# Kernel optimization log

Measured on AMD Instinct MI355X. Metric: run time of the kernel, lower is better.

Reference implementation:

```python
import jax, jax.numpy as jnp
import numpy as np

B, K, D_MODEL = 4, 8400, 512
H, Q, V = 8, 64, 64
WIN, PAD = 168, 42
STEP = WIN - 2 * PAD  # 84


def setup_inputs() -> dict:
    key = jax.random.key(0)
    ks = jax.random.split(key, 11)
    s = 0.02
    return {
        "query": jax.random.normal(ks[0], (B, K, D_MODEL), jnp.float32),
        "key":   jax.random.normal(ks[1], (B, K, D_MODEL), jnp.float32),
        "value": jax.random.normal(ks[2], (B, K, D_MODEL), jnp.float32),
        "W_q": jax.random.normal(ks[3], (D_MODEL, Q * H), jnp.float32) * s,
        "b_q": jax.random.normal(ks[4], (Q * H,), jnp.float32) * s,
        "W_k": jax.random.normal(ks[5], (D_MODEL, Q * H), jnp.float32) * s,
        "b_k": jax.random.normal(ks[6], (Q * H,), jnp.float32) * s,
        "W_v": jax.random.normal(ks[7], (D_MODEL, V * H), jnp.float32) * s,
        "b_v": jax.random.normal(ks[8], (V * H,), jnp.float32) * s,
        "W_o": jax.random.normal(ks[9], (H * V, D_MODEL), jnp.float32) * s,
        "b_o": jax.random.normal(ks[10], (D_MODEL,), jnp.float32) * s,
    }


def _heads(x, d):
    # torch.cat(x.chunk(h, -1), dim=0): (B, Kp, h*d) -> (h*B, Kp, d), head-major
    b, kp, _ = x.shape
    return jnp.transpose(x.reshape(b, kp, H, d), (2, 0, 1, 3)).reshape(H * b, kp, d)


def reference(query, key, value, W_q, b_q, W_k, b_k, W_v, b_v, W_o, b_o):
    b = query.shape[0]
    # replicate padding along time axis
    pad = lambda x: jnp.pad(x, ((0, 0), (PAD, PAD), (0, 0)), mode="edge")
    qp, kp_, vp = pad(query), pad(key), pad(value)

    Qh = _heads(qp @ W_q + b_q, Q)   # (hB, Kp, Q)
    Kh = _heads(kp_ @ W_k + b_k, Q)
    Vh = _heads(vp @ W_v + b_v, V)

    n_win = K // STEP  # 100
    widx = jnp.arange(n_win)[:, None] * STEP + jnp.arange(WIN)[None, :]
    Qw = Qh[:, widx, :]
    Kw = Kh[:, widx, :]
    Vw = Vh[:, widx, :]

    scores = jnp.einsum("bnwq,bnxq->bnwx", Qw, Kw) / np.sqrt(WIN).astype(np.float32)
    tri = jnp.triu(jnp.ones((WIN, WIN), bool), 1)  # subsequent mask
    scores = jnp.where(tri, -jnp.inf, scores)
    attn_w = jax.nn.softmax(scores, axis=-1)
    attn = jnp.einsum("bnwx,bnxv->bnwv", attn_w, Vw)

    attn = attn[:, :, PAD:WIN - PAD, :]                      # crop padding
    attn = attn.reshape(H, b, n_win * STEP, V)               # (h, B, K, V)
    heads = jnp.transpose(attn, (1, 2, 0, 3)).reshape(b, K, H * V)
    return heads @ W_o + b_o
```

## Files before the change

kernel.cpp:

```cpp
#include <hip/hip_runtime.h>
#include <hip/hip_bf16.h>
#include <stdint.h>

#define BATCH 4
#define SEQ   8400
#define DM    512
#define KP    8484
#define NWIN  100
#define STEP_ 84
#define PAD_  42
#define NKEY  126
#define MROWS 33600

typedef __attribute__((ext_vector_type(8))) short short8;
typedef __attribute__((ext_vector_type(4))) float float4v;
typedef __attribute__((ext_vector_type(4))) unsigned short ushort4v;

#define MFMA16 __builtin_amdgcn_mfma_f32_16x16x32_bf16

__device__ __forceinline__ unsigned short f2bf(float f) {
    union { float f; unsigned u; } v; v.f = f;
    return (unsigned short)((v.u + 0x7FFFu + ((v.u >> 16) & 1u)) >> 16);
}
__device__ __forceinline__ unsigned short bfc(float f) {
    __hip_bfloat16 h = __float2bfloat16(f);
    union { __hip_bfloat16 h; unsigned short u; } v; v.h = h;
    return v.u;
}

typedef __attribute__((address_space(1))) const unsigned int as1_cu32;
typedef __attribute__((address_space(3))) unsigned int as3_u32;
__device__ __forceinline__ void gload16(const void* g, void* l) {
    __builtin_amdgcn_global_load_lds((as1_cu32*)g, (as3_u32*)l, 16, 0, 0);
}

__global__ __launch_bounds__(256) void kprep(const float* __restrict__ Wq,
                                             const float* __restrict__ Wk,
                                             const float* __restrict__ Wv,
                                             const float* __restrict__ Wo,
                                             unsigned short* __restrict__ Wt) {
    const float* src = blockIdx.z == 0 ? Wq : blockIdx.z == 1 ? Wk
                     : blockIdx.z == 2 ? Wv : Wo;
    unsigned short* dst = Wt + (size_t)blockIdx.z * DM * DM;
    __shared__ float t[64][65];
    int c = threadIdx.x & 63, r4 = threadIdx.x >> 6;
    int kb = blockIdx.x * 64, nb = blockIdx.y * 64;
    for (int i = 0; i < 16; i++) {
        int r = r4 * 16 + i;
        t[r][c] = src[(size_t)(kb + r) * DM + nb + c];
    }
    __syncthreads();
    for (int i = 0; i < 16; i++) {
        int r = r4 * 16 + i;
        dst[(size_t)(nb + r) * DM + kb + c] = f2bf(t[c][r]);
    }
}

__global__ __launch_bounds__(256, 2) void kproj(const float* __restrict__ q,
                                                const float* __restrict__ k,
                                                const float* __restrict__ v,
                                                const unsigned short* __restrict__ Wt,
                                                const float* __restrict__ bq,
                                                const float* __restrict__ bk,
                                                const float* __restrict__ bv,
                                                unsigned short* __restrict__ Qb,
                                                unsigned short* __restrict__ Kb,
                                                unsigned short* __restrict__ VT) {
    int mt = blockIdx.x, z = blockIdx.y;
    int ten = z >> 2, b = z & 3;
    const float* A = (ten == 0 ? q : ten == 1 ? k : v) + (size_t)b * SEQ * DM;
    const unsigned short* W = Wt + (size_t)ten * DM * DM;
    const float* bias = ten == 0 ? bq : ten == 1 ? bk : bv;
    float scale = ten == 0 ? 0.07715167498104595f : 1.f;
    int m0 = mt * 64;

    __shared__ __align__(16) char lds[81920];

    int tid = threadIdx.x, lane = tid & 63, wc = tid >> 6;
    int l15 = lane & 15, g = lane >> 4;

    float4v acc[4][8];
#pragma unroll
    for (int i = 0; i < 4; i++)
#pragma unroll
        for (int j = 0; j < 8; j++) { float4v zz = {0.f,0.f,0.f,0.f}; acc[i][j] = zz; }

    for (int kt = 0; kt < 8; kt++) {
#pragma unroll
        for (int it = 0; it < 4; it++) {
            int c = it * 256 + tid;
            int r = c >> 4;
            int c4 = (c & 15) ^ (r & 15);
            int p = m0 + r; if (p > KP - 1) p = KP - 1;
            int row = p - PAD_; row = row < 0 ? 0 : (row > SEQ - 1 ? SEQ - 1 : row);
            gload16(A + (size_t)row * DM + kt * 64 + c4 * 4,
                    lds + it * 4096 + wc * 1024);
        }
#pragma unroll
        for (int it = 0; it < 16; it++) {
            int c = it * 256 + tid;
            int r = c >> 3;
            int kg = (c & 7) ^ (r & 7);
            gload16(W + (size_t)r * DM + kt * 64 + kg * 8,
                    lds + 16384 + it * 4096 + wc * 1024);
        }
        __syncthreads();
#pragma unroll
        for (int ks = 0; ks < 2; ks++) {
            short8 af[4];
#pragma unroll
            for (int i = 0; i < 4; i++) {
                int r = i * 16 + l15;
                int c4a = (ks * 4 + g) * 2;
                float4v f0 = *(const float4v*)(lds + r * 256 + ((c4a ^ l15) << 4));
                float4v f1 = *(const float4v*)(lds + r * 256 + (((c4a + 1) ^ l15) << 4));
                short8 hv;
                hv[0] = (short)bfc(f0.x); hv[1] = (short)bfc(f0.y);
                hv[2] = (short)bfc(f0.z); hv[3] = (short)bfc(f0.w);
                hv[4] = (short)bfc(f1.x); hv[5] = (short)bfc(f1.y);
                hv[6] = (short)bfc(f1.z); hv[7] = (short)bfc(f1.w);
                af[i] = hv;
            }
            short8 bfr[8];
#pragma unroll
            for (int j = 0; j < 8; j++) {
                int r = wc * 128 + j * 16 + l15;
                int kg = ks * 4 + g;
                bfr[j] = *(const short8*)(lds + 16384 + r * 128 + ((kg ^ (r & 7)) << 4));
            }
#pragma unroll
            for (int i = 0; i < 4; i++)
#pragma unroll
                for (int j = 0; j < 8; j++)
                    acc[i][j] = MFMA16(af[i], bfr[j], acc[i][j], 0, 0, 0);
        }
        __syncthreads();
    }

    if (ten <= 1) {
        unsigned short* Ol = (unsigned short*)lds;
#pragma unroll
        for (int j = 0; j < 8; j++) {
            int n = wc * 128 + j * 16 + l15;
            float bval = bias[n];
#pragma unroll
            for (int i = 0; i < 4; i++) {
                float4v vv = acc[i][j];
#pragma unroll
                for (int r = 0; r < 4; r++)
                    Ol[(i * 16 + g * 4 + r) * 520 + n] = f2bf((vv[r] + bval) * scale);
            }
        }
        __syncthreads();
        unsigned short* O = ten == 0 ? Qb : Kb;
        for (int c = tid; c < 4096; c += 256) {
            int row = c >> 6, n8 = c & 63;
            int p = m0 + row;
            if (p < KP) {
                int h = n8 >> 3, ch = n8 & 7;
                *(short8*)(O + ((size_t)(h * BATCH + b) * KP + p) * 64 + ch * 8) =
                    *(const short8*)(Ol + row * 520 + n8 * 8);
            }
        }
    } else {
#pragma unroll
        for (int j = 0; j < 8; j++) {
            int n = wc * 128 + j * 16 + l15;
            float bval = bias[n];
            int h = n >> 6, d = n & 63;
            unsigned short* base = VT + ((size_t)(h * BATCH + b) * 64 + d) * KP;
#pragma unroll
            for (int i = 0; i < 4; i++) {
                int p = m0 + i * 16 + g * 4;
                if (p <= KP - 4) {
                    float4v vv = acc[i][j];
                    ushort4v wv;
                    wv[0] = f2bf(vv.x + bval); wv[1] = f2bf(vv.y + bval);
                    wv[2] = f2bf(vv.z + bval); wv[3] = f2bf(vv.w + bval);
                    *(ushort4v*)(base + p) = wv;
                }
            }
        }
    }
}

__global__ __launch_bounds__(384) void kattn(const unsigned short* __restrict__ Qb,
                                             const unsigned short* __restrict__ Kb,
                                             const unsigned short* __restrict__ VT,
                                             unsigned short* __restrict__ attn) {
    int win = blockIdx.x, hb = blockIdx.y;
    int h = hb >> 2, b = hb & 3;
    const unsigned short* Qg = Qb + (size_t)hb * KP * 64;
    const unsigned short* Kg = Kb + (size_t)hb * KP * 64;
    const unsigned short* Vt = VT + (size_t)hb * 64 * KP;
    int p0 = win * STEP_;

    __shared__ __align__(16) char lds[69632];

    int tid = threadIdx.x, lane = tid & 63, f = tid >> 6;
    int l15 = lane & 15, g = lane >> 4;

#pragma unroll
    for (int it = 0; it < 5; it++) {
        int base = it * 384 + f * 64;
        if (base < 768) {
            int c = base + lane;
            int qi = c >> 3, kg = (c & 7) ^ (qi & 7);
            gload16(Qg + (size_t)(p0 + PAD_ + qi) * 64 + kg * 8, lds + base * 16);
        } else if (base < 1792) {
            int c = base + lane - 768;
            int x = c >> 3, kg = (c & 7) ^ (x & 7);
            gload16(Kg + (size_t)(p0 + x) * 64 + kg * 8, lds + base * 16);
        }
    }
    for (int c = tid; c < 2048; c += 384) {
        int d = c >> 5, c2 = c & 31;
        ushort4v wv = *(const ushort4v*)(Vt + (size_t)d * KP + p0 + c2 * 4);
        int cx = c2 >> 1;
        *(ushort4v*)(lds + 28672 + d * 256 + (((cx ^ (d & 7)) << 4) | ((c2 & 1) * 8))) = wv;
    }
    __syncthreads();

    short8 bq2[2];
    {
        int r = f * 16 + l15;
#pragma unroll
        for (int ks = 0; ks < 2; ks++) {
            int kg = ks * 4 + g;
            bq2[ks] = *(const short8*)(lds + r * 128 + ((kg ^ (r & 7)) << 4));
        }
    }
    float4v st[8];
#pragma unroll
    for (int xf = 0; xf < 8; xf++) {
        float4v zz = {0.f,0.f,0.f,0.f}; st[xf] = zz;
#pragma unroll
        for (int ks = 0; ks < 2; ks++) {
            int r = xf * 16 + l15;
            int kg = ks * 4 + g;
            short8 a = *(const short8*)(lds + 12288 + r * 128 + ((kg ^ (r & 7)) << 4));
            st[xf] = MFMA16(a, bq2[ks], st[xf], 0, 0, 0);
        }
    }

    int w_abs = PAD_ + f * 16 + l15;
    int w_eff = w_abs > 125 ? 125 : w_abs;
    float mx = -1e30f;
#pragma unroll
    for (int xf = 0; xf < 8; xf++)
#pragma unroll
        for (int r = 0; r < 4; r++) {
            int x = xf * 16 + g * 4 + r;
            float vv = st[xf][r];
            if (x > w_eff) vv = -1e30f;
            st[xf][r] = vv;
            mx = fmaxf(mx, vv);
        }
    mx = fmaxf(mx, __shfl_xor(mx, 16));
    mx = fmaxf(mx, __shfl_xor(mx, 32));
    float s = 0.f;
#pragma unroll
    for (int xf = 0; xf < 8; xf++)
#pragma unroll
        for (int r = 0; r < 4; r++) {
            float e = __expf(st[xf][r] - mx);
            st[xf][r] = e;
            s += e;
        }
    s += __shfl_xor(s, 16);
    s += __shfl_xor(s, 32);
    float inv = 1.f / s;

    {
        int qi = f * 16 + l15;
#pragma unroll
        for (int xf = 0; xf < 8; xf++) {
            ushort4v pw;
#pragma unroll
            for (int r = 0; r < 4; r++) pw[r] = f2bf(st[xf][r] * inv);
            int xc = 2 * xf + (g >> 1);
            *(ushort4v*)(lds + 45056 + qi * 256 + ((xc ^ (qi & 7)) << 4) + (g & 1) * 8) = pw;
        }
    }
    __syncthreads();

    float4v pv[4];
#pragma unroll
    for (int j = 0; j < 4; j++) { float4v zz = {0.f,0.f,0.f,0.f}; pv[j] = zz; }
    int qi = f * 16 + l15;
#pragma unroll
    for (int g2 = 0; g2 < 4; g2++) {
        int xc = g2 * 4 + g;
        short8 a = *(const short8*)(lds + 45056 + qi * 256 + ((xc ^ (qi & 7)) << 4));
#pragma unroll
        for (int j = 0; j < 4; j++) {
            int d = j * 16 + l15;
            short8 bvv = *(const short8*)(lds + 28672 + d * 256 + ((xc ^ (d & 7)) << 4));
            pv[j] = MFMA16(a, bvv, pv[j], 0, 0, 0);
        }
    }

    unsigned short* Ol = (unsigned short*)lds;
#pragma unroll
    for (int j = 0; j < 4; j++) {
        int d = j * 16 + l15;
#pragma unroll
        for (int r = 0; r < 4; r++) {
            int qq = f * 16 + g * 4 + r;
            int byte = qq * 128 + ((((d >> 3) ^ (qq & 7))) << 4) + (d & 7) * 2;
            *(unsigned short*)((char*)Ol + byte) = f2bf(pv[j][r]);
        }
    }
    __syncthreads();
    for (int c = tid; c < 672; c += 384) {
        int qq = c >> 3, ch = c & 7;
        short8 hv = *(const short8*)((char*)Ol + qq * 128 + ((ch ^ (qq & 7)) << 4));
        size_t off = ((size_t)(b * SEQ + win * STEP_ + qq) * DM) + h * 64 + ch * 8;
        *(short8*)(attn + off) = hv;
    }
}

__global__ __launch_bounds__(256, 2) void kout(const unsigned short* __restrict__ Ab,
                                               const unsigned short* __restrict__ W,
                                               const float* __restrict__ bias,
                                               float* __restrict__ Out) {
    int m0 = blockIdx.x * 64;
    __shared__ __align__(16) char lds[73728];
    int tid = threadIdx.x, lane = tid & 63, wc = tid >> 6;
    int l15 = lane & 15, g = lane >> 4;

    float4v acc[4][8];
#pragma unroll
    for (int i = 0; i < 4; i++)
#pragma unroll
        for (int j = 0; j < 8; j++) { float4v zz = {0.f,0.f,0.f,0.f}; acc[i][j] = zz; }

    for (int kt = 0; kt < 8; kt++) {
#pragma unroll
        for (int it = 0; it < 2; it++) {
            int c = it * 256 + tid;
            int r = c >> 3;
            int kg = (c & 7) ^ (r & 7);
            gload16(Ab + (size_t)(m0 + r) * DM + kt * 64 + kg * 8,
                    lds + it * 4096 + wc * 1024);
        }
#pragma unroll
        for (int it = 0; it < 16; it++) {
            int c = it * 256 + tid;
            int r = c >> 3;
            int kg = (c & 7) ^ (r & 7);
            gload16(W + (size_t)r * DM + kt * 64 + kg * 8,
                    lds + 8192 + it * 4096 + wc * 1024);
        }
        __syncthreads();
#pragma unroll
        for (int ks = 0; ks < 2; ks++) {
            short8 af[4];
#pragma unroll
            for (int i = 0; i < 4; i++) {
                int r = i * 16 + l15;
                int kg = ks * 4 + g;
                af[i] = *(const short8*)(lds + r * 128 + ((kg ^ (r & 7)) << 4));
            }
            short8 bfr[8];
#pragma unroll
            for (int j = 0; j < 8; j++) {
                int r = wc * 128 + j * 16 + l15;
                int kg = ks * 4 + g;
                bfr[j] = *(const short8*)(lds + 8192 + r * 128 + ((kg ^ (r & 7)) << 4));
            }
#pragma unroll
            for (int i = 0; i < 4; i++)
#pragma unroll
                for (int j = 0; j < 8; j++)
                    acc[i][j] = MFMA16(af[i], bfr[j], acc[i][j], 0, 0, 0);
        }
        __syncthreads();
    }
#pragma unroll
    for (int j = 0; j < 8; j++) {
        int n = wc * 128 + j * 16 + l15;
        float bv = bias[n];
#pragma unroll
        for (int i = 0; i < 4; i++) {
            float4v vv = acc[i][j];
#pragma unroll
            for (int r = 0; r < 4; r++) {
                int m = m0 + i * 16 + g * 4 + r;
                Out[(size_t)m * DM + n] = vv[r] + bv;
            }
        }
    }
}

extern "C" void kernel_launch(void* const* d_in, const int* in_sizes, int n_in,
                              void* d_out, int out_size, void* d_ws, size_t ws_size,
                              hipStream_t stream) {
    const float* q  = (const float*)d_in[0];
    const float* k  = (const float*)d_in[1];
    const float* v  = (const float*)d_in[2];
    const float* Wq = (const float*)d_in[3];
    const float* bq = (const float*)d_in[4];
    const float* Wk = (const float*)d_in[5];
    const float* bk = (const float*)d_in[6];
    const float* Wv = (const float*)d_in[7];
    const float* bv = (const float*)d_in[8];
    const float* Wo = (const float*)d_in[9];
    const float* bo = (const float*)d_in[10];

    const size_t WT_ELEMS  = (size_t)4 * DM * DM;
    const size_t QKV_ELEMS = (size_t)32 * KP * 64;
    const size_t ATT_ELEMS = (size_t)MROWS * DM;
    size_t need = (WT_ELEMS + 3 * QKV_ELEMS + ATT_ELEMS) * 2;
    if (ws_size < need) return;

    unsigned short* Wt = (unsigned short*)d_ws;
    unsigned short* Qb = Wt + WT_ELEMS;
    unsigned short* Kb = Qb + QKV_ELEMS;
    unsigned short* VT = Kb + QKV_ELEMS;
    unsigned short* Ab = VT + QKV_ELEMS;

    kprep<<<dim3(8, 8, 4), dim3(256), 0, stream>>>(Wq, Wk, Wv, Wo, Wt);
    kproj<<<dim3(133, 12), dim3(256), 0, stream>>>(q, k, v, Wt, bq, bk, bv,
                                                   Qb, Kb, VT);
    kattn<<<dim3(NWIN, 32), dim3(384), 0, stream>>>(Qb, Kb, VT, Ab);
    kout<<<dim3(525), dim3(256), 0, stream>>>(Ab, Wt + 3 * DM * DM, bo,
                                              (float*)d_out);
}
```

Baseline: 229.5 us.

## Double-buffer LDS staging in projection GEMMs with async prefetch of next K-tile

Both the QKV projection kernel and the output projection kernel change from a single-buffered K loop (64-wide tiles, load then sync then compute) to a double-buffered pipeline with 32-wide K tiles. The next tile's global-to-LDS loads are issued before computing the current one, and partial vmcnt waits plus raw s_barrier replace full __syncthreads. The aim is to hide global load latency behind MFMA work. In exchange, K-steps double to 16, the LDS swizzle layout changes, and row clamping plus an output guard are added in kout.

```diff
diff --git a/kernel.cpp b/kernel.cpp
--- a/kernel.cpp
+++ b/kernel.cpp
@@ -85,56 +85,65 @@
 #pragma unroll
         for (int j = 0; j < 8; j++) { float4v zz = {0.f,0.f,0.f,0.f}; acc[i][j] = zz; }
 
-    for (int kt = 0; kt < 8; kt++) {
-#pragma unroll
-        for (int it = 0; it < 4; it++) {
+    auto stageA = [&](int kt, int buf) {
+#pragma unroll
+        for (int it = 0; it < 2; it++) {
             int c = it * 256 + tid;
-            int r = c >> 4;
-            int c4 = (c & 15) ^ (r & 15);
+            int r = c >> 3;
+            int pos = (c & 7) ^ (r & 7);
             int p = m0 + r; if (p > KP - 1) p = KP - 1;
             int row = p - PAD_; row = row < 0 ? 0 : (row > SEQ - 1 ? SEQ - 1 : row);
-            gload16(A + (size_t)row * DM + kt * 64 + c4 * 4,
-                    lds + it * 4096 + wc * 1024);
-        }
-#pragma unroll
-        for (int it = 0; it < 16; it++) {
+            gload16(A + (size_t)row * DM + kt * 32 + pos * 4,
+                    lds + buf * 8192 + (it * 256 + wc * 64) * 16);
+        }
+    };
+    auto stageB = [&](int kt, int buf) {
+#pragma unroll
+        for (int it = 0; it < 8; it++) {
             int c = it * 256 + tid;
-            int r = c >> 3;
-            int kg = (c & 7) ^ (r & 7);
-            gload16(W + (size_t)r * DM + kt * 64 + kg * 8,
-                    lds + 16384 + it * 4096 + wc * 1024);
-        }
-        __syncthreads();
-#pragma unroll
-        for (int ks = 0; ks < 2; ks++) {
-            short8 af[4];
-#pragma unroll
-            for (int i = 0; i < 4; i++) {
-                int r = i * 16 + l15;
-                int c4a = (ks * 4 + g) * 2;
-                float4v f0 = *(const float4v*)(lds + r * 256 + ((c4a ^ l15) << 4));
-                float4v f1 = *(const float4v*)(lds + r * 256 + (((c4a + 1) ^ l15) << 4));
-                short8 hv;
-                hv[0] = (short)bfc(f0.x); hv[1] = (short)bfc(f0.y);
-                hv[2] = (short)bfc(f0.z); hv[3] = (short)bfc(f0.w);
-                hv[4] = (short)bfc(f1.x); hv[5] = (short)bfc(f1.y);
-                hv[6] = (short)bfc(f1.z); hv[7] = (short)bfc(f1.w);
-                af[i] = hv;
-            }
-            short8 bfr[8];
-#pragma unroll
-            for (int j = 0; j < 8; j++) {
-                int r = wc * 128 + j * 16 + l15;
-                int kg = ks * 4 + g;
-                bfr[j] = *(const short8*)(lds + 16384 + r * 128 + ((kg ^ (r & 7)) << 4));
-            }
-#pragma unroll
-            for (int i = 0; i < 4; i++)
-#pragma unroll
-                for (int j = 0; j < 8; j++)
-                    acc[i][j] = MFMA16(af[i], bfr[j], acc[i][j], 0, 0, 0);
-        }
-        __syncthreads();
+            int r = c >> 2;
+            int pos = (c & 3) ^ ((r >> 1) & 3);
+            gload16(W + (size_t)r * DM + kt * 32 + pos * 8,
+                    lds + 16384 + buf * 32768 + (it * 256 + wc * 64) * 16);
+        }
+    };
+
+    stageA(0, 0); stageB(0, 0);
+#pragma unroll
+    for (int t = 0; t < 16; ++t) {
+        int cur = t & 1;
+        if (t < 15) { stageA(t + 1, cur ^ 1); stageB(t + 1, cur ^ 1); }
+        if (t < 15) asm volatile("s_waitcnt vmcnt(10)" ::: "memory");
+        else        asm volatile("s_waitcnt vmcnt(0)" ::: "memory");
+        __builtin_amdgcn_s_barrier();
+        __builtin_amdgcn_sched_barrier(0);
+        const char* Ab_ = lds + cur * 8192;
+        const char* Bb_ = lds + 16384 + cur * 32768;
+        short8 af[4];
+#pragma unroll
+        for (int i = 0; i < 4; i++) {
+            int ra = i * 16 + l15;
+            float4v f0 = *(const float4v*)(Ab_ + ra * 128 + (((2 * g) ^ (ra & 7)) << 4));
+            float4v f1 = *(const float4v*)(Ab_ + ra * 128 + (((2 * g + 1) ^ (ra & 7)) << 4));
+            short8 hv;
+            hv[0] = (short)bfc(f0.x); hv[1] = (short)bfc(f0.y);
+            hv[2] = (short)bfc(f0.z); hv[3] = (short)bfc(f0.w);
+            hv[4] = (short)bfc(f1.x); hv[5] = (short)bfc(f1.y);
+            hv[6] = (short)bfc(f1.z); hv[7] = (short)bfc(f1.w);
+            af[i] = hv;
+        }
+        short8 bfr[8];
+#pragma unroll
+        for (int j = 0; j < 8; j++) {
+            int rb = wc * 128 + j * 16 + l15;
+            bfr[j] = *(const short8*)(Bb_ + rb * 64 + ((g ^ ((rb >> 1) & 3)) << 4));
+        }
+#pragma unroll
+        for (int i = 0; i < 4; i++)
+#pragma unroll
+            for (int j = 0; j < 8; j++)
+                acc[i][j] = MFMA16(af[i], bfr[j], acc[i][j], 0, 0, 0);
+        __builtin_amdgcn_s_barrier();
     }
 
     if (ten <= 1) {
@@ -335,47 +344,54 @@
 #pragma unroll
         for (int j = 0; j < 8; j++) { float4v zz = {0.f,0.f,0.f,0.f}; acc[i][j] = zz; }
 
-    for (int kt = 0; kt < 8; kt++) {
-#pragma unroll
-        for (int it = 0; it < 2; it++) {
+    auto stageA = [&](int kt, int buf) {
+        int c = tid;
+        int r = c >> 2;
+        int pos = (c & 3) ^ ((r >> 1) & 3);
+        int row = m0 + r; if (row > MROWS - 1) row = MROWS - 1;
+        gload16(Ab + (size_t)row * DM + kt * 32 + pos * 8,
+                lds + buf * 4096 + (wc * 64) * 16);
+    };
+    auto stageB = [&](int kt, int buf) {
+#pragma unroll
+        for (int it = 0; it < 8; it++) {
             int c = it * 256 + tid;
-            int r = c >> 3;
-            int kg = (c & 7) ^ (r & 7);
-            gload16(Ab + (size_t)(m0 + r) * DM + kt * 64 + kg * 8,
-                    lds + it * 4096 + wc * 1024);
-        }
-#pragma unroll
-        for (int it = 0; it < 16; it++) {
-            int c = it * 256 + tid;
-            int r = c >> 3;
-            int kg = (c & 7) ^ (r & 7);
-            gload16(W + (size_t)r * DM + kt * 64 + kg * 8,
-                    lds + 8192 + it * 4096 + wc * 1024);
-        }
-        __syncthreads();
-#pragma unroll
-        for (int ks = 0; ks < 2; ks++) {
-            short8 af[4];
-#pragma unroll
-            for (int i = 0; i < 4; i++) {
-                int r = i * 16 + l15;
-                int kg = ks * 4 + g;
-                af[i] = *(const short8*)(lds + r * 128 + ((kg ^ (r & 7)) << 4));
-            }
-            short8 bfr[8];
-#pragma unroll
-            for (int j = 0; j < 8; j++) {
-                int r = wc * 128 + j * 16 + l15;
-                int kg = ks * 4 + g;
-                bfr[j] = *(const short8*)(lds + 8192 + r * 128 + ((kg ^ (r & 7)) << 4));
-            }
-#pragma unroll
-            for (int i = 0; i < 4; i++)
-#pragma unroll
-                for (int j = 0; j < 8; j++)
-                    acc[i][j] = MFMA16(af[i], bfr[j], acc[i][j], 0, 0, 0);
-        }
-        __syncthreads();
+            int r = c >> 2;
+            int pos = (c & 3) ^ ((r >> 1) & 3);
+            gload16(W + (size_t)r * DM + kt * 32 + pos * 8,
+                    lds + 8192 + buf * 32768 + (it * 256 + wc * 64) * 16);
+        }
+    };
+
+    stageA(0, 0); stageB(0, 0);
+#pragma unroll
+    for (int t = 0; t < 16; ++t) {
+        int cur = t & 1;
+        if (t < 15) { stageA(t + 1, cur ^ 1); stageB(t + 1, cur ^ 1); }
+        if (t < 15) asm volatile("s_waitcnt vmcnt(9)" ::: "memory");
+        else        asm volatile("s_waitcnt vmcnt(0)" ::: "memory");
+        __builtin_amdgcn_s_barrier();
+        __builtin_amdgcn_sched_barrier(0);
+        const char* Ab_ = lds + cur * 4096;
+        const char* Bb_ = lds + 8192 + cur * 32768;
+        short8 af[4];
+#pragma unroll
+        for (int i = 0; i < 4; i++) {
+            int ra = i * 16 + l15;
+            af[i] = *(const short8*)(Ab_ + ra * 64 + ((g ^ ((ra >> 1) & 3)) << 4));
+        }
+        short8 bfr[8];
+#pragma unroll
+        for (int j = 0; j < 8; j++) {
+            int rb = wc * 128 + j * 16 + l15;
+            bfr[j] = *(const short8*)(Bb_ + rb * 64 + ((g ^ ((rb >> 1) & 3)) << 4));
+        }
+#pragma unroll
+        for (int i = 0; i < 4; i++)
+#pragma unroll
+            for (int j = 0; j < 8; j++)
+                acc[i][j] = MFMA16(af[i], bfr[j], acc[i][j], 0, 0, 0);
+        __builtin_amdgcn_s_barrier();
     }
 #pragma unroll
     for (int j = 0; j < 8; j++) {
@@ -387,7 +403,7 @@
 #pragma unroll
             for (int r = 0; r < 4; r++) {
                 int m = m0 + i * 16 + g * 4 + r;
-                Out[(size_t)m * DM + n] = vv[r] + bv;
+                if (m < MROWS) Out[(size_t)m * DM + n] = vv[r] + bv;
             }
         }
     }
```

Result: slower. 271.0 us (+18.1%).

## Retile projection GEMMs to 128x128 tiles with 2x2 wave layout

Applied to the files above, without the earlier changes.

Both the QKV projection and output projection GEMMs switch from 64-row by full-512-column tiles to 128x128 tiles, splitting N across a new grid dimension. Each wave now computes a 64x64 sub-tile. In kproj, the fp32 activations are converted to bf16 once when staged into shared memory, replacing per-fragment conversion from an fp32 LDS tile. This shrinks LDS use and register accumulators so more blocks fit per CU. The cost is that each A tile is now re-read by four N-blocks, and the padded last M tile adds some wasted work.

```diff
diff --git a/kernel.cpp b/kernel.cpp
--- a/kernel.cpp
+++ b/kernel.cpp
@@ -56,82 +56,90 @@
     }
 }
 
-__global__ __launch_bounds__(256, 2) void kproj(const float* __restrict__ q,
-                                                const float* __restrict__ k,
-                                                const float* __restrict__ v,
-                                                const unsigned short* __restrict__ Wt,
-                                                const float* __restrict__ bq,
-                                                const float* __restrict__ bk,
-                                                const float* __restrict__ bv,
-                                                unsigned short* __restrict__ Qb,
-                                                unsigned short* __restrict__ Kb,
-                                                unsigned short* __restrict__ VT) {
-    int mt = blockIdx.x, z = blockIdx.y;
+__global__ __launch_bounds__(256) void kproj(const float* __restrict__ q,
+                                             const float* __restrict__ k,
+                                             const float* __restrict__ v,
+                                             const unsigned short* __restrict__ Wt,
+                                             const float* __restrict__ bq,
+                                             const float* __restrict__ bk,
+                                             const float* __restrict__ bv,
+                                             unsigned short* __restrict__ Qb,
+                                             unsigned short* __restrict__ Kb,
+                                             unsigned short* __restrict__ VT) {
+    int mt = blockIdx.x, nt = blockIdx.y, z = blockIdx.z;
     int ten = z >> 2, b = z & 3;
     const float* A = (ten == 0 ? q : ten == 1 ? k : v) + (size_t)b * SEQ * DM;
     const unsigned short* W = Wt + (size_t)ten * DM * DM;
     const float* bias = ten == 0 ? bq : ten == 1 ? bk : bv;
     float scale = ten == 0 ? 0.07715167498104595f : 1.f;
-    int m0 = mt * 64;
-
-    __shared__ __align__(16) char lds[81920];
-
-    int tid = threadIdx.x, lane = tid & 63, wc = tid >> 6;
+    int m0 = mt * 128, n0 = nt * 128;
+
+    __shared__ __align__(16) char lds[34816];
+    char* Al = lds;
+    char* Bl = lds + 16384;
+
+    int tid = threadIdx.x, lane = tid & 63, w = tid >> 6;
+    int wm = (w >> 1) * 64, wn = (w & 1) * 64;
     int l15 = lane & 15, g = lane >> 4;
 
-    float4v acc[4][8];
+    int ar4 = tid >> 2;
+    int ac = tid & 3;
+    int c0 = ac * 2;
+
+    float4v acc[4][4];
 #pragma unroll
     for (int i = 0; i < 4; i++)
 #pragma unroll
-        for (int j = 0; j < 8; j++) { float4v zz = {0.f,0.f,0.f,0.f}; acc[i][j] = zz; }
+        for (int j = 0; j < 4; j++) { float4v zz = {0.f,0.f,0.f,0.f}; acc[i][j] = zz; }
 
     for (int kt = 0; kt < 8; kt++) {
 #pragma unroll
         for (int it = 0; it < 4; it++) {
-            int c = it * 256 + tid;
-            int r = c >> 4;
-            int c4 = (c & 15) ^ (r & 15);
-            int p = m0 + r; if (p > KP - 1) p = KP - 1;
-            int row = p - PAD_; row = row < 0 ? 0 : (row > SEQ - 1 ? SEQ - 1 : row);
-            gload16(A + (size_t)row * DM + kt * 64 + c4 * 4,
-                    lds + it * 4096 + wc * 1024);
-        }
-#pragma unroll
-        for (int it = 0; it < 16; it++) {
             int c = it * 256 + tid;
             int r = c >> 3;
             int kg = (c & 7) ^ (r & 7);
-            gload16(W + (size_t)r * DM + kt * 64 + kg * 8,
-                    lds + 16384 + it * 4096 + wc * 1024);
+            gload16(W + (size_t)(n0 + r) * DM + kt * 64 + kg * 8, Bl + c * 16);
+        }
+#pragma unroll
+        for (int it = 0; it < 2; it++) {
+            int rr = it * 64 + ar4;
+            int p = m0 + rr;
+            int row = p - PAD_; row = row < 0 ? 0 : (row > SEQ - 1 ? SEQ - 1 : row);
+            const float* src = A + (size_t)row * DM + kt * 64 + ac * 16;
+            float4v f0 = *(const float4v*)(src);
+            float4v f1 = *(const float4v*)(src + 4);
+            float4v f2 = *(const float4v*)(src + 8);
+            float4v f3 = *(const float4v*)(src + 12);
+            short8 h0, h1;
+            h0[0] = (short)bfc(f0.x); h0[1] = (short)bfc(f0.y);
+            h0[2] = (short)bfc(f0.z); h0[3] = (short)bfc(f0.w);
+            h0[4] = (short)bfc(f1.x); h0[5] = (short)bfc(f1.y);
+            h0[6] = (short)bfc(f1.z); h0[7] = (short)bfc(f1.w);
+            h1[0] = (short)bfc(f2.x); h1[1] = (short)bfc(f2.y);
+            h1[2] = (short)bfc(f2.z); h1[3] = (short)bfc(f2.w);
+            h1[4] = (short)bfc(f3.x); h1[5] = (short)bfc(f3.y);
+            h1[6] = (short)bfc(f3.z); h1[7] = (short)bfc(f3.w);
+            *(short8*)(Al + rr * 128 + ((c0 ^ (rr & 7)) << 4)) = h0;
+            *(short8*)(Al + rr * 128 + (((c0 + 1) ^ (rr & 7)) << 4)) = h1;
         }
         __syncthreads();
 #pragma unroll
         for (int ks = 0; ks < 2; ks++) {
-            short8 af[4];
+            short8 af[4], bfr[4];
 #pragma unroll
             for (int i = 0; i < 4; i++) {
-                int r = i * 16 + l15;
-                int c4a = (ks * 4 + g) * 2;
-                float4v f0 = *(const float4v*)(lds + r * 256 + ((c4a ^ l15) << 4));
-                float4v f1 = *(const float4v*)(lds + r * 256 + (((c4a + 1) ^ l15) << 4));
-                short8 hv;
-                hv[0] = (short)bfc(f0.x); hv[1] = (short)bfc(f0.y);
-                hv[2] = (short)bfc(f0.z); hv[3] = (short)bfc(f0.w);
-                hv[4] = (short)bfc(f1.x); hv[5] = (short)bfc(f1.y);
-                hv[6] = (short)bfc(f1.z); hv[7] = (short)bfc(f1.w);
-                af[i] = hv;
-            }
-            short8 bfr[8];
-#pragma unroll
-            for (int j = 0; j < 8; j++) {
-                int r = wc * 128 + j * 16 + l15;
-                int kg = ks * 4 + g;
-                bfr[j] = *(const short8*)(lds + 16384 + r * 128 + ((kg ^ (r & 7)) << 4));
+                int r = wm + i * 16 + l15, kg = ks * 4 + g;
+                af[i] = *(const short8*)(Al + r * 128 + ((kg ^ (r & 7)) << 4));
+            }
+#pragma unroll
+            for (int j = 0; j < 4; j++) {
+                int r = wn + j * 16 + l15, kg = ks * 4 + g;
+                bfr[j] = *(const short8*)(Bl + r * 128 + ((kg ^ (r & 7)) << 4));
             }
 #pragma unroll
             for (int i = 0; i < 4; i++)
 #pragma unroll
-                for (int j = 0; j < 8; j++)
+                for (int j = 0; j < 4; j++)
                     acc[i][j] = MFMA16(af[i], bfr[j], acc[i][j], 0, 0, 0);
         }
         __syncthreads();
@@ -140,38 +148,40 @@
     if (ten <= 1) {
         unsigned short* Ol = (unsigned short*)lds;
 #pragma unroll
-        for (int j = 0; j < 8; j++) {
-            int n = wc * 128 + j * 16 + l15;
-            float bval = bias[n];
+        for (int j = 0; j < 4; j++) {
+            int nl = wn + j * 16 + l15;
+            float bval = bias[n0 + nl];
 #pragma unroll
             for (int i = 0; i < 4; i++) {
                 float4v vv = acc[i][j];
 #pragma unroll
                 for (int r = 0; r < 4; r++)
-                    Ol[(i * 16 + g * 4 + r) * 520 + n] = f2bf((vv[r] + bval) * scale);
+                    Ol[(wm + i * 16 + g * 4 + r) * 136 + nl] =
+                        f2bf((vv[r] + bval) * scale);
             }
         }
         __syncthreads();
         unsigned short* O = ten == 0 ? Qb : Kb;
-        for (int c = tid; c < 4096; c += 256) {
-            int row = c >> 6, n8 = c & 63;
+        int hbase = n0 >> 6;
+        for (int c = tid; c < 2048; c += 256) {
+            int row = c >> 4, chunk = c & 15;
             int p = m0 + row;
             if (p < KP) {
-                int h = n8 >> 3, ch = n8 & 7;
+                int h = hbase + (chunk >> 3), ch = chunk & 7;
                 *(short8*)(O + ((size_t)(h * BATCH + b) * KP + p) * 64 + ch * 8) =
-                    *(const short8*)(Ol + row * 520 + n8 * 8);
+                    *(const short8*)(Ol + row * 136 + chunk * 8);
             }
         }
     } else {
 #pragma unroll
-        for (int j = 0; j < 8; j++) {
-            int n = wc * 128 + j * 16 + l15;
+        for (int j = 0; j < 4; j++) {
+            int n = n0 + wn + j * 16 + l15;
             float bval = bias[n];
             int h = n >> 6, d = n & 63;
             unsigned short* base = VT + ((size_t)(h * BATCH + b) * 64 + d) * KP;
 #pragma unroll
             for (int i = 0; i < 4; i++) {
-                int p = m0 + i * 16 + g * 4;
+                int p = m0 + wm + i * 16 + g * 4;
                 if (p <= KP - 4) {
                     float4v vv = acc[i][j];
                     ushort4v wv;
@@ -320,74 +330,73 @@
     }
 }
 
-__global__ __launch_bounds__(256, 2) void kout(const unsigned short* __restrict__ Ab,
-                                               const unsigned short* __restrict__ W,
-                                               const float* __restrict__ bias,
-                                               float* __restrict__ Out) {
-    int m0 = blockIdx.x * 64;
-    __shared__ __align__(16) char lds[73728];
-    int tid = threadIdx.x, lane = tid & 63, wc = tid >> 6;
+__global__ __launch_bounds__(256) void kout(const unsigned short* __restrict__ Ab,
+                                            const unsigned short* __restrict__ W,
+                                            const float* __restrict__ bias,
+                                            float* __restrict__ Out) {
+    int m0 = blockIdx.x * 128, n0 = blockIdx.y * 128;
+    __shared__ __align__(16) char lds[32768];
+    char* Al = lds;
+    char* Bl = lds + 16384;
+    int tid = threadIdx.x, lane = tid & 63, w = tid >> 6;
+    int wm = (w >> 1) * 64, wn = (w & 1) * 64;
     int l15 = lane & 15, g = lane >> 4;
 
-    float4v acc[4][8];
+    float4v acc[4][4];
 #pragma unroll
     for (int i = 0; i < 4; i++)
 #pragma unroll
-        for (int j = 0; j < 8; j++) { float4v zz = {0.f,0.f,0.f,0.f}; acc[i][j] = zz; }
+        for (int j = 0; j < 4; j++) { float4v zz = {0.f,0.f,0.f,0.f}; acc[i][j] = zz; }
 
     for (int kt = 0; kt < 8; kt++) {
 #pragma unroll
-        for (int it = 0; it < 2; it++) {
+        for (int it = 0; it < 4; it++) {
             int c = it * 256 + tid;
             int r = c >> 3;
             int kg = (c & 7) ^ (r & 7);
-            gload16(Ab + (size_t)(m0 + r) * DM + kt * 64 + kg * 8,
-                    lds + it * 4096 + wc * 1024);
-        }
-#pragma unroll
-        for (int it = 0; it < 16; it++) {
+            int row = m0 + r; if (row > MROWS - 1) row = MROWS - 1;
+            gload16(Ab + (size_t)row * DM + kt * 64 + kg * 8, Al + c * 16);
+        }
+#pragma unroll
+        for (int it = 0; it < 4; it++) {
             int c = it * 256 + tid;
             int r = c >> 3;
             int kg = (c & 7) ^ (r & 7);
-            gload16(W + (size_t)r * DM + kt * 64 + kg * 8,
-                    lds + 8192 + it * 4096 + wc * 1024);
+            gload16(W + (size_t)(n0 + r) * DM + kt * 64 + kg * 8, Bl + c * 16);
         }
         __syncthreads();
 #pragma unroll
         for (int ks = 0; ks < 2; ks++) {
-            short8 af[4];
+            short8 af[4], bfr[4];
 #pragma unroll
             for (int i = 0; i < 4; i++) {
-                int r = i * 16 + l15;
-                int kg = ks * 4 + g;
-                af[i] = *(const short8*)(lds + r * 128 + ((kg ^ (r & 7)) << 4));
-            }
-            short8 bfr[8];
-#pragma unroll
-            for (int j = 0; j < 8; j++) {
-                int r = wc * 128 + j * 16 + l15;
-                int kg = ks * 4 + g;
-                bfr[j] = *(const short8*)(lds + 8192 + r * 128 + ((kg ^ (r & 7)) << 4));
+                int r = wm + i * 16 + l15, kg = ks * 4 + g;
+                af[i] = *(const short8*)(Al + r * 128 + ((kg ^ (r & 7)) << 4));
+            }
+#pragma unroll
+            for (int j = 0; j < 4; j++) {
+                int r = wn + j * 16 + l15, kg = ks * 4 + g;
+                bfr[j] = *(const short8*)(Bl + r * 128 + ((kg ^ (r & 7)) << 4));
             }
 #pragma unroll
             for (int i = 0; i < 4; i++)
 #pragma unroll
-                for (int j = 0; j < 8; j++)
+                for (int j = 0; j < 4; j++)
                     acc[i][j] = MFMA16(af[i], bfr[j], acc[i][j], 0, 0, 0);
         }
         __syncthreads();
     }
 #pragma unroll
-    for (int j = 0; j < 8; j++) {
-        int n = wc * 128 + j * 16 + l15;
+    for (int j = 0; j < 4; j++) {
+        int n = n0 + wn + j * 16 + l15;
         float bv = bias[n];
 #pragma unroll
         for (int i = 0; i < 4; i++) {
             float4v vv = acc[i][j];
 #pragma unroll
             for (int r = 0; r < 4; r++) {
-                int m = m0 + i * 16 + g * 4 + r;
-                Out[(size_t)m * DM + n] = vv[r] + bv;
+                int m = m0 + wm + i * 16 + g * 4 + r;
+                if (m < MROWS) Out[(size_t)m * DM + n] = vv[r] + bv;
             }
         }
     }
@@ -421,9 +430,9 @@
     unsigned short* Ab = VT + QKV_ELEMS;
 
     kprep<<<dim3(8, 8, 4), dim3(256), 0, stream>>>(Wq, Wk, Wv, Wo, Wt);
-    kproj<<<dim3(133, 12), dim3(256), 0, stream>>>(q, k, v, Wt, bq, bk, bv,
-                                                   Qb, Kb, VT);
+    kproj<<<dim3(67, 4, 12), dim3(256), 0, stream>>>(q, k, v, Wt, bq, bk, bv,
+                                                     Qb, Kb, VT);
     kattn<<<dim3(NWIN, 32), dim3(384), 0, stream>>>(Qb, Kb, VT, Ab);
-    kout<<<dim3(525), dim3(256), 0, stream>>>(Ab, Wt + 3 * DM * DM, bo,
-                                              (float*)d_out);
-}
+    kout<<<dim3(263, 4), dim3(256), 0, stream>>>(Ab, Wt + 3 * DM * DM, bo,
+                                                 (float*)d_out);
+}
```

Measured after the change: 299.6 us. 1.31x slower.
